# Performance work log

Hardware: AMD Instinct MI355X
Metric: run time of the kernel (lower is better)

Reference implementation:

```python
import jax, jax.numpy as jnp
import numpy as np

WS = (8, 8)            # window_size
NUM_HEADS = 8


def _rel_pos_index():
    # Faithful to the torch buffer construction (meshgrid indexing='ij').
    ch, cw = np.arange(WS[0]), np.arange(WS[1])
    coords = np.stack(np.meshgrid(ch, cw, indexing='ij')).reshape(2, -1)  # (2, N)
    rel = coords[:, :, None] - coords[:, None, :]                          # (2, N, N)
    rel = rel.transpose(1, 2, 0).copy()                                    # (N, N, 2)
    rel[..., 0] += WS[0] - 1
    rel[..., 1] += WS[1] - 1
    rel[..., 0] *= 2 * WS[1] - 1
    return jnp.asarray(rel.sum(-1))                                        # (N, N) int


def setup_inputs() -> dict:
    key = jax.random.key(0)
    ks = jax.random.split(key, 7)
    B_, C, N, nW = 4096, 256, 64, 4096  # B_ = batch(1) * num_windows(4096)
    return {
        "x": jax.random.normal(ks[0], (B_, C, N), jnp.float32),
        "mask": jax.random.normal(ks[1], (nW, N, N), jnp.float32),
        "qkv_w": jax.random.normal(ks[2], (3 * C, C), jnp.float32) * 0.05,
        "qkv_b": jax.random.normal(ks[3], (3 * C,), jnp.float32) * 0.02,
        "proj_w": jax.random.normal(ks[4], (C, C), jnp.float32) * 0.05,
        "proj_b": jax.random.normal(ks[5], (C,), jnp.float32) * 0.02,
        "bias_table": jax.random.normal(ks[6], ((2 * WS[0] - 1) * (2 * WS[1] - 1), NUM_HEADS), jnp.float32) * 0.02,
    }


def reference(x, mask, qkv_w, qkv_b, proj_w, proj_b, bias_table):
    B_, C, N = x.shape
    H = NUM_HEADS
    hd = C // H
    scale = hd ** -0.5

    # Conv1d kernel_size=1 == linear over the channel dim.
    qkv = jnp.einsum('bcn,dc->bdn', x, qkv_w) + qkv_b[None, :, None]   # (B_, 3C, N)
    qkv = qkv.reshape(B_, 3, H, hd, N)
    q, k, v = qkv[:, 0], qkv[:, 1], qkv[:, 2]                          # (B_, H, hd, N)

    attn = jnp.einsum('bhdn,bhdm->bhnm', q * scale, k)                 # (B_, H, N, N)

    rpi = _rel_pos_index()                                              # (N, N)
    bias = bias_table[rpi]                                              # (N, N, H) gather
    attn = attn + jnp.transpose(bias, (2, 0, 1))[None]                  # (B_, H, N, N)

    nW = mask.shape[0]
    attn = (attn.reshape(B_ // nW, nW, H, N, N) + mask[None, :, None]).reshape(B_, H, N, N)
    attn = jax.nn.softmax(attn, axis=-1)

    out = jnp.einsum('bhnm,bhdm->bnhd', attn, v).reshape(B_, N, C)      # (B_, N, C)
    return jnp.einsum('bnc,dc->bnd', out, proj_w) + proj_b              # (B_, N, C)
```

## Files before the change

kernel.cpp:

```cpp
#include <hip/hip_runtime.h>

typedef __bf16 bf16_t;
typedef bf16_t bf16x8 __attribute__((ext_vector_type(8)));
typedef bf16_t bf16x4 __attribute__((ext_vector_type(4)));
typedef float  f32x4  __attribute__((ext_vector_type(4)));

#define NWIN 4096
#define CDIM 256
#define NTOK 64
#define NH   8

#define OFF_MASK  40960
#define LDS_BYTES 58368

__device__ __forceinline__ f32x4 mfma16(bf16x8 a, bf16x8 b, f32x4 c) {
    return __builtin_amdgcn_mfma_f32_16x16x32_bf16(a, b, c, 0, 0, 0);
}

template<bool USE_WS>
__device__ __forceinline__ bf16x8 load_wrow(const bf16_t* wb, const float* wf, int row, int c) {
    if constexpr (USE_WS) {
        return *(const bf16x8*)(wb + row * CDIM + c);
    } else {
        const float* ap = wf + row * CDIM + c;
        f32x4 a0 = *(const f32x4*)ap;
        f32x4 a1 = *(const f32x4*)(ap + 4);
        bf16x8 t;
        #pragma unroll
        for (int j = 0; j < 4; ++j) { t[j] = (bf16_t)a0[j]; t[j + 4] = (bf16_t)a1[j]; }
        return t;
    }
}

template<bool USE_WS>
__launch_bounds__(512, 4)
__global__ void win_attn_kernel(const float* __restrict__ x,
                                const float* __restrict__ mask,
                                const float* __restrict__ qkv_w,
                                const float* __restrict__ qkv_b,
                                const float* __restrict__ proj_w,
                                const float* __restrict__ proj_b,
                                const float* __restrict__ bias_table,
                                const bf16_t* __restrict__ qkv_wb,
                                const bf16_t* __restrict__ proj_wb,
                                const float* __restrict__ bias_pre,
                                float* __restrict__ out)
{
    __shared__ __attribute__((aligned(16))) unsigned char smem[LDS_BYTES];
    bf16_t* xs       = (bf16_t*)smem;
    bf16_t* o_lds    = (bf16_t*)smem;
    float*  mask_lds = (float*)(smem + OFF_MASK);

    const int b    = blockIdx.x;
    const int tid  = threadIdx.x;
    const int w    = tid >> 6;
    const int lane = tid & 63;
    const int quad = lane >> 4;
    const int l15  = lane & 15;
    bf16_t* buf0 = (bf16_t*)(smem + w * 5120);

    {
        const float* xb = x + (size_t)b * (CDIM * NTOK);
        #pragma unroll
        for (int cb = 0; cb < 4; ++cb) {
            const int c0 = cb * 64 + w * 8;
            float v[8];
            #pragma unroll
            for (int j = 0; j < 8; ++j) v[j] = xb[(c0 + j) * 64 + lane];
            bf16x8 t;
            #pragma unroll
            for (int j = 0; j < 8; ++j) t[j] = (bf16_t)v[j];
            *(bf16x8*)(xs + lane * 264 + c0) = t;
        }
        const float* mb = mask + (size_t)b * (NTOK * NTOK);
        #pragma unroll
        for (int it = 0; it < 2; ++it) {
            int e = (it * 512 + tid) * 4;
            int n = e >> 6, m = e & 63;
            f32x4 mv = *(const f32x4*)(mb + e);
            *(f32x4*)(mask_lds + n * 68 + m) = mv;
        }
    }
    __syncthreads();

    const int h = w;
    const float scale = 0.17677669529663687f;

    bf16x4 kpk[2][4];
    bf16x4 vpk[4][2];

    {
        f32x4 acc[4][2];
        #pragma unroll
        for (int ct = 0; ct < 4; ++ct)
            #pragma unroll
            for (int rtl = 0; rtl < 2; ++rtl) acc[ct][rtl] = (f32x4){0.f,0.f,0.f,0.f};

        const int r0 = 512 + h * 32 + l15;
        bf16x8 a0 = load_wrow<USE_WS>(qkv_wb, qkv_w, r0,      quad * 8);
        bf16x8 a1 = load_wrow<USE_WS>(qkv_wb, qkv_w, r0 + 16, quad * 8);
        #pragma unroll 1
        for (int kk = 0; kk < 8; ++kk) {
            const int c0 = kk * 32;
            const int c1 = ((kk + 1) & 7) * 32 + quad * 8;
            bf16x8 n0 = load_wrow<USE_WS>(qkv_wb, qkv_w, r0,      c1);
            bf16x8 n1 = load_wrow<USE_WS>(qkv_wb, qkv_w, r0 + 16, c1);
            bf16x8 bfr[4];
            #pragma unroll
            for (int ct = 0; ct < 4; ++ct)
                bfr[ct] = *(const bf16x8*)(xs + (ct * 16 + l15) * 264 + c0 + quad * 8);
            #pragma unroll
            for (int ct = 0; ct < 4; ++ct) {
                acc[ct][0] = mfma16(bfr[ct], a0, acc[ct][0]);
                acc[ct][1] = mfma16(bfr[ct], a1, acc[ct][1]);
            }
            a0 = n0; a1 = n1;
        }
        #pragma unroll
        for (int rtl = 0; rtl < 2; ++rtl) {
            float bv = qkv_b[512 + h * 32 + rtl * 16 + l15];
            #pragma unroll
            for (int ct = 0; ct < 4; ++ct)
                #pragma unroll
                for (int r = 0; r < 4; ++r) vpk[ct][rtl][r] = (bf16_t)(acc[ct][rtl][r] + bv);
        }
    }
    {
        f32x4 acc[2][4];
        #pragma unroll
        for (int rtl = 0; rtl < 2; ++rtl)
            #pragma unroll
            for (int ct = 0; ct < 4; ++ct) acc[rtl][ct] = (f32x4){0.f,0.f,0.f,0.f};

        const int r0 = 256 + h * 32 + l15;
        bf16x8 a0 = load_wrow<USE_WS>(qkv_wb, qkv_w, r0,      quad * 8);
        bf16x8 a1 = load_wrow<USE_WS>(qkv_wb, qkv_w, r0 + 16, quad * 8);
        #pragma unroll 1
        for (int kk = 0; kk < 8; ++kk) {
            const int c0 = kk * 32;
            const int c1 = ((kk + 1) & 7) * 32 + quad * 8;
            bf16x8 n0 = load_wrow<USE_WS>(qkv_wb, qkv_w, r0,      c1);
            bf16x8 n1 = load_wrow<USE_WS>(qkv_wb, qkv_w, r0 + 16, c1);
            bf16x8 bfr[4];
            #pragma unroll
            for (int ct = 0; ct < 4; ++ct)
                bfr[ct] = *(const bf16x8*)(xs + (ct * 16 + l15) * 264 + c0 + quad * 8);
            #pragma unroll
            for (int ct = 0; ct < 4; ++ct) {
                acc[0][ct] = mfma16(a0, bfr[ct], acc[0][ct]);
                acc[1][ct] = mfma16(a1, bfr[ct], acc[1][ct]);
            }
            a0 = n0; a1 = n1;
        }
        #pragma unroll
        for (int rtl = 0; rtl < 2; ++rtl) {
            f32x4 b4 = *(const f32x4*)(qkv_b + 256 + h * 32 + rtl * 16 + quad * 4);
            #pragma unroll
            for (int ct = 0; ct < 4; ++ct)
                #pragma unroll
                for (int r = 0; r < 4; ++r) kpk[rtl][ct][r] = (bf16_t)(acc[rtl][ct][r] + b4[r]);
        }
    }
    f32x4 qacc[2][4];
    {
        #pragma unroll
        for (int rtl = 0; rtl < 2; ++rtl)
            #pragma unroll
            for (int ct = 0; ct < 4; ++ct) qacc[rtl][ct] = (f32x4){0.f,0.f,0.f,0.f};

        const int r0 = h * 32 + l15;
        bf16x8 a0 = load_wrow<USE_WS>(qkv_wb, qkv_w, r0,      quad * 8);
        bf16x8 a1 = load_wrow<USE_WS>(qkv_wb, qkv_w, r0 + 16, quad * 8);
        #pragma unroll 1
        for (int kk = 0; kk < 8; ++kk) {
            const int c0 = kk * 32;
            const int c1 = ((kk + 1) & 7) * 32 + quad * 8;
            bf16x8 n0 = load_wrow<USE_WS>(qkv_wb, qkv_w, r0,      c1);
            bf16x8 n1 = load_wrow<USE_WS>(qkv_wb, qkv_w, r0 + 16, c1);
            bf16x8 bfr[4];
            #pragma unroll
            for (int ct = 0; ct < 4; ++ct)
                bfr[ct] = *(const bf16x8*)(xs + (ct * 16 + l15) * 264 + c0 + quad * 8);
            #pragma unroll
            for (int ct = 0; ct < 4; ++ct) {
                qacc[0][ct] = mfma16(a0, bfr[ct], qacc[0][ct]);
                qacc[1][ct] = mfma16(a1, bfr[ct], qacc[1][ct]);
            }
            a0 = n0; a1 = n1;
        }
    }
    __syncthreads();

    #pragma unroll
    for (int rtl = 0; rtl < 2; ++rtl) {
        f32x4 b4 = *(const f32x4*)(qkv_b + h * 32 + rtl * 16 + quad * 4);
        #pragma unroll
        for (int ct = 0; ct < 4; ++ct) {
            bf16x4 pk;
            #pragma unroll
            for (int r = 0; r < 4; ++r) pk[r] = (bf16_t)((qacc[rtl][ct][r] + b4[r]) * scale);
            *(bf16x4*)(buf0 + (ct * 16 + l15) * 40 + rtl * 16 + quad * 4) = pk;
        }
    }
    bf16x8 qa[4];
    #pragma unroll
    for (int nt = 0; nt < 4; ++nt)
        qa[nt] = *(const bf16x8*)(buf0 + (nt * 16 + l15) * 40 + quad * 8);

    #pragma unroll
    for (int rtl = 0; rtl < 2; ++rtl)
        #pragma unroll
        for (int ct = 0; ct < 4; ++ct)
            *(bf16x4*)(buf0 + (ct * 16 + l15) * 40 + rtl * 16 + quad * 4) = kpk[rtl][ct];
    bf16x8 kb[4];
    #pragma unroll
    for (int mt = 0; mt < 4; ++mt)
        kb[mt] = *(const bf16x8*)(buf0 + (mt * 16 + l15) * 40 + quad * 8);

    #pragma unroll
    for (int rtl = 0; rtl < 2; ++rtl)
        #pragma unroll
        for (int ct = 0; ct < 4; ++ct)
            *(bf16x4*)(buf0 + (rtl * 16 + l15) * 72 + ct * 16 + quad * 4) = vpk[ct][rtl];

    float inv[4];
    bf16x4 ppk[4][4];
    {
        const int qhi = quad >> 1, qlo = quad & 1;
        const int nwv = (l15 & 7) + 7 - 4 * qlo;
        const int nh_ = l15 >> 3;
        #pragma unroll
        for (int nt = 0; nt < 4; ++nt) {
            f32x4 scol[4];
            #pragma unroll
            for (int mt = 0; mt < 4; ++mt)
                scol[mt] = mfma16(kb[mt], qa[nt], (f32x4){0.f,0.f,0.f,0.f});
            const int n = nt * 16 + l15;
            if constexpr (USE_WS) {
                const float* bh = bias_pre + (h << 12) + n * 64;
                #pragma unroll
                for (int mt = 0; mt < 4; ++mt) {
                    f32x4 bv = *(const f32x4*)(bh + mt * 16 + quad * 4);
                    f32x4 mv = *(const f32x4*)(mask_lds + n * 68 + mt * 16 + quad * 4);
                    scol[mt] += bv + mv;
                }
            } else {
                #pragma unroll
                for (int mt = 0; mt < 4; ++mt) {
                    f32x4 mv = *(const f32x4*)(mask_lds + n * 68 + mt * 16 + quad * 4);
                    int base = (nt * 2 + nh_ - 2 * mt - qhi + 7) * 15 + nwv;
                    #pragma unroll
                    for (int r = 0; r < 4; ++r)
                        scol[mt][r] += bias_table[(base - r) * NH + h] + mv[r];
                }
            }
            float mx = scol[0][0];
            #pragma unroll
            for (int mt = 0; mt < 4; ++mt)
                #pragma unroll
                for (int r = 0; r < 4; ++r) mx = fmaxf(mx, scol[mt][r]);
            mx = fmaxf(mx, __shfl_xor(mx, 16, 64));
            mx = fmaxf(mx, __shfl_xor(mx, 32, 64));
            float s = 0.f;
            #pragma unroll
            for (int mt = 0; mt < 4; ++mt)
                #pragma unroll
                for (int r = 0; r < 4; ++r) {
                    float e = __expf(scol[mt][r] - mx);
                    ppk[mt][nt][r] = (bf16_t)e;
                    s += e;
                }
            s += __shfl_xor(s, 16, 64);
            s += __shfl_xor(s, 32, 64);
            inv[nt] = __builtin_amdgcn_rcpf(s);
        }
    }

    bf16x8 vb[2][2];
    #pragma unroll
    for (int dt = 0; dt < 2; ++dt)
        #pragma unroll
        for (int ch = 0; ch < 2; ++ch)
            vb[dt][ch] = *(const bf16x8*)(buf0 + (dt * 16 + l15) * 72 + ch * 32 + quad * 8);

    f32x4 oaccT[2][4];
    #pragma unroll
    for (int dt = 0; dt < 2; ++dt)
        #pragma unroll
        for (int nt = 0; nt < 4; ++nt) oaccT[dt][nt] = (f32x4){0.f,0.f,0.f,0.f};

    #pragma unroll
    for (int ch = 0; ch < 2; ++ch) {
        #pragma unroll
        for (int mt2 = 0; mt2 < 2; ++mt2) {
            #pragma unroll
            for (int nt = 0; nt < 4; ++nt)
                *(bf16x4*)(buf0 + (nt * 16 + l15) * 40 + mt2 * 16 + quad * 4) = ppk[2 * ch + mt2][nt];
        }
        #pragma unroll
        for (int nt = 0; nt < 4; ++nt) {
            bf16x8 pb = *(const bf16x8*)(buf0 + (nt * 16 + l15) * 40 + quad * 8);
            #pragma unroll
            for (int dt = 0; dt < 2; ++dt)
                oaccT[dt][nt] = mfma16(vb[dt][ch], pb, oaccT[dt][nt]);
        }
    }
    __syncthreads();

    #pragma unroll
    for (int dt = 0; dt < 2; ++dt)
        #pragma unroll
        for (int nt = 0; nt < 4; ++nt) {
            bf16x4 pk;
            #pragma unroll
            for (int r = 0; r < 4; ++r) pk[r] = (bf16_t)(oaccT[dt][nt][r] * inv[nt]);
            *(bf16x4*)(o_lds + (nt * 16 + l15) * 264 + h * 32 + dt * 16 + quad * 4) = pk;
        }
    __syncthreads();

    {
        f32x4 yacc[2][4];
        #pragma unroll
        for (int rt = 0; rt < 2; ++rt)
            #pragma unroll
            for (int ct = 0; ct < 4; ++ct) yacc[rt][ct] = (f32x4){0.f,0.f,0.f,0.f};

        const int e0r = w * 32 + l15;
        bf16x8 a0 = load_wrow<USE_WS>(proj_wb, proj_w, e0r,      quad * 8);
        bf16x8 a1 = load_wrow<USE_WS>(proj_wb, proj_w, e0r + 16, quad * 8);
        #pragma unroll 1
        for (int kk = 0; kk < 8; ++kk) {
            const int c0 = kk * 32;
            const int c1 = ((kk + 1) & 7) * 32 + quad * 8;
            bf16x8 n0 = load_wrow<USE_WS>(proj_wb, proj_w, e0r,      c1);
            bf16x8 n1 = load_wrow<USE_WS>(proj_wb, proj_w, e0r + 16, c1);
            bf16x8 bfr[4];
            #pragma unroll
            for (int ct = 0; ct < 4; ++ct)
                bfr[ct] = *(const bf16x8*)(o_lds + (ct * 16 + l15) * 264 + c0 + quad * 8);
            #pragma unroll
            for (int ct = 0; ct < 4; ++ct) {
                yacc[0][ct] = mfma16(a0, bfr[ct], yacc[0][ct]);
                yacc[1][ct] = mfma16(a1, bfr[ct], yacc[1][ct]);
            }
            a0 = n0; a1 = n1;
        }
        float* ob = out + (size_t)b * (NTOK * CDIM);
        #pragma unroll
        for (int rt = 0; rt < 2; ++rt) {
            int e0 = w * 32 + rt * 16 + quad * 4;
            f32x4 pb4 = *(const f32x4*)(proj_b + e0);
            #pragma unroll
            for (int ct = 0; ct < 4; ++ct) {
                int n = ct * 16 + l15;
                f32x4 r = yacc[rt][ct] + pb4;
                *(f32x4*)(ob + n * 256 + e0) = r;
            }
        }
    }
}

__global__ void cvt_weights(const float* __restrict__ qkv_w,
                            const float* __restrict__ proj_w,
                            const float* __restrict__ bias_table,
                            bf16_t* __restrict__ qkv_wb,
                            bf16_t* __restrict__ proj_wb,
                            float* __restrict__ bias_pre)
{
    int i = blockIdx.x * 256 + threadIdx.x;
    if (i < 65536) {
        int base = i * 4;
        const float* src; bf16_t* dst;
        if (base < 196608) { src = qkv_w + base; dst = qkv_wb + base; }
        else { base -= 196608; src = proj_w + base; dst = proj_wb + base; }
        f32x4 v = *(const f32x4*)src;
        bf16x4 o;
        #pragma unroll
        for (int j = 0; j < 4; ++j) o[j] = (bf16_t)v[j];
        *(bf16x4*)dst = o;
    } else {
        int base = (i - 65536) * 4;
        int h = base >> 12, n = (base >> 6) & 63, m0 = base & 63;
        f32x4 o;
        #pragma unroll
        for (int j = 0; j < 4; ++j) {
            int m = m0 + j;
            int idx = ((n >> 3) - (m >> 3) + 7) * 15 + ((n & 7) - (m & 7) + 7);
            o[j] = bias_table[idx * NH + h];
        }
        *(f32x4*)(bias_pre + base) = o;
    }
}

extern "C" void kernel_launch(void* const* d_in, const int* in_sizes, int n_in,
                              void* d_out, int out_size, void* d_ws, size_t ws_size,
                              hipStream_t stream) {
    const float* x          = (const float*)d_in[0];
    const float* mask       = (const float*)d_in[1];
    const float* qkv_w      = (const float*)d_in[2];
    const float* qkv_b      = (const float*)d_in[3];
    const float* proj_w     = (const float*)d_in[4];
    const float* proj_b     = (const float*)d_in[5];
    const float* bias_table = (const float*)d_in[6];
    float* out = (float*)d_out;

    const size_t ws_needed = 524288 + 524288;
    if (ws_size >= ws_needed) {
        bf16_t* qkv_wb  = (bf16_t*)d_ws;
        bf16_t* proj_wb = qkv_wb + 196608;
        float*  bias_pre = (float*)((unsigned char*)d_ws + 524288);
        cvt_weights<<<384, 256, 0, stream>>>(qkv_w, proj_w, bias_table, qkv_wb, proj_wb, bias_pre);
        win_attn_kernel<true><<<NWIN, 512, 0, stream>>>(
            x, mask, qkv_w, qkv_b, proj_w, proj_b, bias_table, qkv_wb, proj_wb, bias_pre, out);
    } else {
        win_attn_kernel<false><<<NWIN, 512, 0, stream>>>(
            x, mask, qkv_w, qkv_b, proj_w, proj_b, bias_table, nullptr, nullptr, nullptr, out);
    }
}
```

Before: 747.6 us.

## Replace padded LDS layouts with XOR-swizzled layouts and stage K separately

```diff
diff --git a/kernel.cpp b/kernel.cpp
--- a/kernel.cpp
+++ b/kernel.cpp
@@ -10,8 +10,9 @@
 #define NTOK 64
 #define NH   8
 
-#define OFF_MASK  40960
-#define LDS_BYTES 58368
+#define OFF_KST  32768
+#define OFF_MASK 65536
+#define LDS_BYTES 81920
 
 __device__ __forceinline__ f32x4 mfma16(bf16x8 a, bf16x8 b, f32x4 c) {
     return __builtin_amdgcn_mfma_f32_16x16x32_bf16(a, b, c, 0, 0, 0);
@@ -47,9 +48,6 @@
                                 float* __restrict__ out)
 {
     __shared__ __attribute__((aligned(16))) unsigned char smem[LDS_BYTES];
-    bf16_t* xs       = (bf16_t*)smem;
-    bf16_t* o_lds    = (bf16_t*)smem;
-    float*  mask_lds = (float*)(smem + OFF_MASK);
 
     const int b    = blockIdx.x;
     const int tid  = threadIdx.x;
@@ -57,7 +55,8 @@
     const int lane = tid & 63;
     const int quad = lane >> 4;
     const int l15  = lane & 15;
-    bf16_t* buf0 = (bf16_t*)(smem + w * 5120);
+    unsigned char* buf0 = smem + w * 4096;
+    unsigned char* kst  = smem + OFF_KST + w * 4096;
 
     {
         const float* xb = x + (size_t)b * (CDIM * NTOK);
@@ -70,7 +69,7 @@
             bf16x8 t;
             #pragma unroll
             for (int j = 0; j < 8; ++j) t[j] = (bf16_t)v[j];
-            *(bf16x8*)(xs + lane * 264 + c0) = t;
+            *(bf16x8*)(smem + lane * 512 + ((c0 * 2) ^ ((lane & 7) << 4))) = t;
         }
         const float* mb = mask + (size_t)b * (NTOK * NTOK);
         #pragma unroll
@@ -78,7 +77,7 @@
             int e = (it * 512 + tid) * 4;
             int n = e >> 6, m = e & 63;
             f32x4 mv = *(const f32x4*)(mb + e);
-            *(f32x4*)(mask_lds + n * 68 + m) = mv;
+            *(f32x4*)(smem + OFF_MASK + n * 256 + ((m * 4) ^ ((n & 7) << 4))) = mv;
         }
     }
     __syncthreads();
@@ -86,7 +85,6 @@
     const int h = w;
     const float scale = 0.17677669529663687f;
 
-    bf16x4 kpk[2][4];
     bf16x4 vpk[4][2];
 
     {
@@ -101,14 +99,16 @@
         bf16x8 a1 = load_wrow<USE_WS>(qkv_wb, qkv_w, r0 + 16, quad * 8);
         #pragma unroll 1
         for (int kk = 0; kk < 8; ++kk) {
-            const int c0 = kk * 32;
+            const int cb = kk * 64 + quad * 16;
             const int c1 = ((kk + 1) & 7) * 32 + quad * 8;
             bf16x8 n0 = load_wrow<USE_WS>(qkv_wb, qkv_w, r0,      c1);
             bf16x8 n1 = load_wrow<USE_WS>(qkv_wb, qkv_w, r0 + 16, c1);
             bf16x8 bfr[4];
             #pragma unroll
-            for (int ct = 0; ct < 4; ++ct)
-                bfr[ct] = *(const bf16x8*)(xs + (ct * 16 + l15) * 264 + c0 + quad * 8);
+            for (int ct = 0; ct < 4; ++ct) {
+                int row = ct * 16 + l15;
+                bfr[ct] = *(const bf16x8*)(smem + row * 512 + (cb ^ ((row & 7) << 4)));
+            }
             #pragma unroll
             for (int ct = 0; ct < 4; ++ct) {
                 acc[ct][0] = mfma16(bfr[ct], a0, acc[ct][0]);
@@ -137,14 +137,16 @@
         bf16x8 a1 = load_wrow<USE_WS>(qkv_wb, qkv_w, r0 + 16, quad * 8);
         #pragma unroll 1
         for (int kk = 0; kk < 8; ++kk) {
-            const int c0 = kk * 32;
+            const int cb = kk * 64 + quad * 16;
             const int c1 = ((kk + 1) & 7) * 32 + quad * 8;
             bf16x8 n0 = load_wrow<USE_WS>(qkv_wb, qkv_w, r0,      c1);
             bf16x8 n1 = load_wrow<USE_WS>(qkv_wb, qkv_w, r0 + 16, c1);
             bf16x8 bfr[4];
             #pragma unroll
-            for (int ct = 0; ct < 4; ++ct)
-                bfr[ct] = *(const bf16x8*)(xs + (ct * 16 + l15) * 264 + c0 + quad * 8);
+            for (int ct = 0; ct < 4; ++ct) {
+                int row = ct * 16 + l15;
+                bfr[ct] = *(const bf16x8*)(smem + row * 512 + (cb ^ ((row & 7) << 4)));
+            }
             #pragma unroll
             for (int ct = 0; ct < 4; ++ct) {
                 acc[0][ct] = mfma16(a0, bfr[ct], acc[0][ct]);
@@ -156,9 +158,13 @@
         for (int rtl = 0; rtl < 2; ++rtl) {
             f32x4 b4 = *(const f32x4*)(qkv_b + 256 + h * 32 + rtl * 16 + quad * 4);
             #pragma unroll
-            for (int ct = 0; ct < 4; ++ct)
-                #pragma unroll
-                for (int r = 0; r < 4; ++r) kpk[rtl][ct][r] = (bf16_t)(acc[rtl][ct][r] + b4[r]);
+            for (int ct = 0; ct < 4; ++ct) {
+                bf16x4 pk;
+                #pragma unroll
+                for (int r = 0; r < 4; ++r) pk[r] = (bf16_t)(acc[rtl][ct][r] + b4[r]);
+                int m = ct * 16 + l15;
+                *(bf16x4*)(kst + m * 64 + ((rtl * 32 + quad * 8) ^ ((m & 3) << 4))) = pk;
+            }
         }
     }
     f32x4 qacc[2][4];
@@ -173,14 +179,16 @@
         bf16x8 a1 = load_wrow<USE_WS>(qkv_wb, qkv_w, r0 + 16, quad * 8);
         #pragma unroll 1
         for (int kk = 0; kk < 8; ++kk) {
-            const int c0 = kk * 32;
+            const int cb = kk * 64 + quad * 16;
             const int c1 = ((kk + 1) & 7) * 32 + quad * 8;
             bf16x8 n0 = load_wrow<USE_WS>(qkv_wb, qkv_w, r0,      c1);
             bf16x8 n1 = load_wrow<USE_WS>(qkv_wb, qkv_w, r0 + 16, c1);
             bf16x8 bfr[4];
             #pragma unroll
-            for (int ct = 0; ct < 4; ++ct)
-                bfr[ct] = *(const bf16x8*)(xs + (ct * 16 + l15) * 264 + c0 + quad * 8);
+            for (int ct = 0; ct < 4; ++ct) {
+                int row = ct * 16 + l15;
+                bfr[ct] = *(const bf16x8*)(smem + row * 512 + (cb ^ ((row & 7) << 4)));
+            }
             #pragma unroll
             for (int ct = 0; ct < 4; ++ct) {
                 qacc[0][ct] = mfma16(a0, bfr[ct], qacc[0][ct]);
@@ -199,29 +207,31 @@
             bf16x4 pk;
             #pragma unroll
             for (int r = 0; r < 4; ++r) pk[r] = (bf16_t)((qacc[rtl][ct][r] + b4[r]) * scale);
-            *(bf16x4*)(buf0 + (ct * 16 + l15) * 40 + rtl * 16 + quad * 4) = pk;
+            int row = ct * 16 + l15;
+            *(bf16x4*)(buf0 + row * 64 + ((rtl * 32 + quad * 8) ^ ((row & 3) << 4))) = pk;
         }
     }
     bf16x8 qa[4];
     #pragma unroll
-    for (int nt = 0; nt < 4; ++nt)
-        qa[nt] = *(const bf16x8*)(buf0 + (nt * 16 + l15) * 40 + quad * 8);
+    for (int nt = 0; nt < 4; ++nt) {
+        int row = nt * 16 + l15;
+        qa[nt] = *(const bf16x8*)(buf0 + row * 64 + ((quad * 16) ^ ((row & 3) << 4)));
+    }
 
     #pragma unroll
     for (int rtl = 0; rtl < 2; ++rtl)
         #pragma unroll
-        for (int ct = 0; ct < 4; ++ct)
-            *(bf16x4*)(buf0 + (ct * 16 + l15) * 40 + rtl * 16 + quad * 4) = kpk[rtl][ct];
+        for (int ct = 0; ct < 4; ++ct) {
+            int d = rtl * 16 + l15;
+            *(bf16x4*)(buf0 + d * 128 + ((ct * 32 + quad * 8) ^ ((d & 7) << 4))) = vpk[ct][rtl];
+        }
+
     bf16x8 kb[4];
     #pragma unroll
-    for (int mt = 0; mt < 4; ++mt)
-        kb[mt] = *(const bf16x8*)(buf0 + (mt * 16 + l15) * 40 + quad * 8);
-
-    #pragma unroll
-    for (int rtl = 0; rtl < 2; ++rtl)
-        #pragma unroll
-        for (int ct = 0; ct < 4; ++ct)
-            *(bf16x4*)(buf0 + (rtl * 16 + l15) * 72 + ct * 16 + quad * 4) = vpk[ct][rtl];
+    for (int mt = 0; mt < 4; ++mt) {
+        int m = mt * 16 + l15;
+        kb[mt] = *(const bf16x8*)(kst + m * 64 + ((quad * 16) ^ ((m & 3) << 4)));
+    }
 
     float inv[4];
     bf16x4 ppk[4][4];
@@ -241,13 +251,15 @@
                 #pragma unroll
                 for (int mt = 0; mt < 4; ++mt) {
                     f32x4 bv = *(const f32x4*)(bh + mt * 16 + quad * 4);
-                    f32x4 mv = *(const f32x4*)(mask_lds + n * 68 + mt * 16 + quad * 4);
+                    f32x4 mv = *(const f32x4*)(smem + OFF_MASK + n * 256 +
+                                               ((mt * 64 + quad * 16) ^ ((n & 7) << 4)));
                     scol[mt] += bv + mv;
                 }
             } else {
                 #pragma unroll
                 for (int mt = 0; mt < 4; ++mt) {
-                    f32x4 mv = *(const f32x4*)(mask_lds + n * 68 + mt * 16 + quad * 4);
+                    f32x4 mv = *(const f32x4*)(smem + OFF_MASK + n * 256 +
+                                               ((mt * 64 + quad * 16) ^ ((n & 7) << 4)));
                     int base = (nt * 2 + nh_ - 2 * mt - qhi + 7) * 15 + nwv;
                     #pragma unroll
                     for (int r = 0; r < 4; ++r)
@@ -280,8 +292,10 @@
     #pragma unroll
     for (int dt = 0; dt < 2; ++dt)
         #pragma unroll
-        for (int ch = 0; ch < 2; ++ch)
-            vb[dt][ch] = *(const bf16x8*)(buf0 + (dt * 16 + l15) * 72 + ch * 32 + quad * 8);
+        for (int ch = 0; ch < 2; ++ch) {
+            int d = dt * 16 + l15;
+            vb[dt][ch] = *(const bf16x8*)(buf0 + d * 128 + ((ch * 64 + quad * 16) ^ ((d & 7) << 4)));
+        }
 
     f32x4 oaccT[2][4];
     #pragma unroll
@@ -294,12 +308,16 @@
         #pragma unroll
         for (int mt2 = 0; mt2 < 2; ++mt2) {
             #pragma unroll
-            for (int nt = 0; nt < 4; ++nt)
-                *(bf16x4*)(buf0 + (nt * 16 + l15) * 40 + mt2 * 16 + quad * 4) = ppk[2 * ch + mt2][nt];
+            for (int nt = 0; nt < 4; ++nt) {
+                int row = nt * 16 + l15;
+                *(bf16x4*)(buf0 + row * 64 + ((mt2 * 32 + quad * 8) ^ ((row & 3) << 4))) =
+                    ppk[2 * ch + mt2][nt];
+            }
         }
         #pragma unroll
         for (int nt = 0; nt < 4; ++nt) {
-            bf16x8 pb = *(const bf16x8*)(buf0 + (nt * 16 + l15) * 40 + quad * 8);
+            int row = nt * 16 + l15;
+            bf16x8 pb = *(const bf16x8*)(buf0 + row * 64 + ((quad * 16) ^ ((row & 3) << 4)));
             #pragma unroll
             for (int dt = 0; dt < 2; ++dt)
                 oaccT[dt][nt] = mfma16(vb[dt][ch], pb, oaccT[dt][nt]);
@@ -314,7 +332,9 @@
             bf16x4 pk;
             #pragma unroll
             for (int r = 0; r < 4; ++r) pk[r] = (bf16_t)(oaccT[dt][nt][r] * inv[nt]);
-            *(bf16x4*)(o_lds + (nt * 16 + l15) * 264 + h * 32 + dt * 16 + quad * 4) = pk;
+            int row = nt * 16 + l15;
+            *(bf16x4*)(smem + row * 512 +
+                       ((h * 64 + dt * 32 + quad * 8) ^ ((row & 7) << 4))) = pk;
         }
     __syncthreads();
 
@@ -330,14 +350,16 @@
         bf16x8 a1 = load_wrow<USE_WS>(proj_wb, proj_w, e0r + 16, quad * 8);
         #pragma unroll 1
         for (int kk = 0; kk < 8; ++kk) {
-            const int c0 = kk * 32;
+            const int cb = kk * 64 + quad * 16;
             const int c1 = ((kk + 1) & 7) * 32 + quad * 8;
             bf16x8 n0 = load_wrow<USE_WS>(proj_wb, proj_w, e0r,      c1);
             bf16x8 n1 = load_wrow<USE_WS>(proj_wb, proj_w, e0r + 16, c1);
             bf16x8 bfr[4];
             #pragma unroll
-            for (int ct = 0; ct < 4; ++ct)
-                bfr[ct] = *(const bf16x8*)(o_lds + (ct * 16 + l15) * 264 + c0 + quad * 8);
+            for (int ct = 0; ct < 4; ++ct) {
+                int row = ct * 16 + l15;
+                bfr[ct] = *(const bf16x8*)(smem + row * 512 + (cb ^ ((row & 7) << 4)));
+            }
             #pragma unroll
             for (int ct = 0; ct < 4; ++ct) {
                 yacc[0][ct] = mfma16(a0, bfr[ct], yacc[0][ct]);
```

New measurement: 733.5 us. About the same (-1.9%).
